# Kernel optimization log

Hardware: AMD Instinct MI355X
Metric: run time of the kernel (lower is better)

Reference implementation:

```python
import jax, jax.numpy as jnp
import numpy as np
from jax import lax

B, T = 16, 128
H, FD = 24, 4          # H hours, FD fourier harmonics
L = 64                 # latent_dim
D = 256                # d_model
NH = 8                 # heads
C = 1 + H * FD         # cont_dim = 97
EPS = 1e-5


def setup_inputs() -> dict:
    key = jax.random.key(0)
    ks = jax.random.split(key, 32)
    r = lambda k, sh, s: (jax.random.normal(k, sh, dtype=jnp.float32) * s)
    z = lambda sh: jnp.zeros(sh, dtype=jnp.float32)
    o = lambda sh: jnp.ones(sh, dtype=jnp.float32)
    return {
        'x_cont': jax.random.normal(ks[0], (B, T, C), dtype=jnp.float32),
        'z0': z((1, 1, L)),                       # learned initial hidden state
        'W_ih': r(ks[1], (L, 1), 0.1),            # RNN input weights
        'W_hh': r(ks[2], (L, L), 0.1),            # RNN recurrent weights
        'b_ih': z((L,)),
        'b_hh': z((L,)),
        'Uf': r(ks[3], (H, FD), 0.01),            # fourier coefficients
        'Wfp': r(ks[4], (L, H), 0.05),            # fourier_proj (L != H)
        'bfp': z((L,)),
        'feat_embed': r(ks[5], (L, D), 0.02),
        'W_in': r(ks[6], (3 * D, D), 0.02),       # MHA in_proj
        'b_in': z((3 * D,)),
        'W_ao': r(ks[7], (D, D), 0.02),           # MHA out_proj
        'b_ao': z((D,)),
        'g1': o((D,)), 'be1': z((D,)),            # ln1
        'W1': r(ks[8], (4 * D, D), 0.02), 'b1': z((4 * D,)),
        'W2': r(ks[9], (D, 4 * D), 0.02), 'b2': z((D,)),
        'g2': o((D,)), 'be2': z((D,)),            # ln2
        'Wop': r(ks[10], (1, D), 0.02), 'bop': z((1,)),   # out_proj d_model->1
        'Wg': r(ks[11], (L, L), 0.05), 'bg': z((L,)),     # gate
        'A': r(ks[12], (H, L), 0.01),
        'c': z((H,)),
    }


def _ln(x, g, b):
    mu = jnp.mean(x, -1, keepdims=True)
    var = jnp.mean(jnp.square(x - mu), -1, keepdims=True)
    return (x - mu) * lax.rsqrt(var + EPS) * g + b


def reference(x_cont, z0, W_ih, W_hh, b_ih, b_hh, Uf, Wfp, bfp, feat_embed,
              W_in, b_in, W_ao, b_ao, g1, be1, W1, b1, W2, b2, g2, be2,
              Wop, bop, Wg, bg, A, c):
    Bb, Tt, Cc = x_cont.shape
    x0 = x_cont[:, :, :1]              # (B,T,1)
    xf = x_cont[:, :, 1:]              # (B,T,H*FD)

    # --- single-layer relu RNN over time ---
    h0 = jnp.broadcast_to(z0[0, 0], (Bb, L))

    def step(h, x_t):                  # x_t: (B,1)
        h = jax.nn.relu(x_t @ W_ih.T + b_ih + h @ W_hh.T + b_hh)
        return h, h

    _, hs = lax.scan(step, h0, jnp.swapaxes(x0, 0, 1))
    h = jnp.swapaxes(hs, 0, 1)         # (B,T,L)

    # --- fourier features ---
    xf_mat = xf.reshape(Bb, Tt, H, FD)
    fourier_h = jnp.einsum('bthf,hf->bth', xf_mat, Uf)   # (B,T,H)
    z = h + fourier_h @ Wfp.T + bfp                      # (B,T,L)

    # --- feature attention: tokens (B*T, L, D) ---
    N = Bb * Tt
    zf = z.reshape(N, L)
    tokens = zf[:, :, None] * feat_embed[None]           # (N,L,D)

    qkv = tokens @ W_in.T + b_in                         # (N,L,3D)
    q, k, v = jnp.split(qkv, 3, axis=-1)
    dh = D // NH
    split_heads = lambda t: t.reshape(N, L, NH, dh).transpose(0, 2, 1, 3)
    q, k, v = split_heads(q), split_heads(k), split_heads(v)
    att = jax.nn.softmax(jnp.einsum('nhqd,nhkd->nhqk', q, k) / np.sqrt(dh), axis=-1)
    ao = jnp.einsum('nhqk,nhkd->nhqd', att, v).transpose(0, 2, 1, 3).reshape(N, L, D)
    ao = ao @ W_ao.T + b_ao

    t1 = _ln(tokens + ao, g1, be1)
    ffn = jax.nn.relu(t1 @ W1.T + b1) @ W2.T + b2
    t2 = _ln(t1 + ffn, g2, be2)
    delta = (t2 @ Wop.T + bop)[..., 0].reshape(Bb, Tt, L)

    gate = jax.nn.sigmoid(z @ Wg.T + bg)
    z_out = z + gate * delta

    o = z_out @ A.T + c                                  # (B,T,H)
    return (o, z_out)
```

## Files before the change

### kernel.cpp

```cpp
#include <hip/hip_runtime.h>

typedef short bf16x8 __attribute__((ext_vector_type(8)));
typedef float f32x4  __attribute__((ext_vector_type(4)));

__device__ __forceinline__ unsigned short f2b(float f){
  union { float f; unsigned u; } v; v.f = f;
  unsigned r = v.u + 0x7FFFu + ((v.u >> 16) & 1u);
  return (unsigned short)(r >> 16);
}
__device__ __forceinline__ float b2f(unsigned short s){
  union { unsigned u; float f; } v; v.u = ((unsigned)s) << 16;
  return v.f;
}
__device__ __forceinline__ unsigned pk2(float lo, float hi){
  unsigned r;
  asm("v_cvt_pk_bf16_f32 %0, %1, %2" : "=v"(r) : "v"(lo), "v"(hi));
  return r;
}

__global__ void k_pre_qkv(const float* __restrict__ FE, const float* __restrict__ W_in,
                          float* __restrict__ Qm, float* __restrict__ Km, float* __restrict__ Vm){
  int id = blockIdx.x*256 + threadIdx.x;
  int part = id >> 14;
  int l = (id >> 8) & 63;
  int d = id & 255;
  const float4* fe = (const float4*)(FE + l*256);
  const float4* wr = (const float4*)(W_in + (part*256 + d)*256);
  float s = 0.f;
  #pragma unroll 8
  for (int k=0;k<64;k++){
    float4 a = fe[k], b = wr[k];
    s += a.x*b.x + a.y*b.y + a.z*b.z + a.w*b.w;
  }
  float* dst = (part==0)?Qm:((part==1)?Km:Vm);
  dst[l*256+d] = s;
}

__global__ void k_pre2(const float* __restrict__ Qm, const float* __restrict__ Km,
                       const float* __restrict__ Vm,
                       const float* __restrict__ b_in, const float* __restrict__ W_ao,
                       const float* __restrict__ b_ao, const float* __restrict__ FE,
                       float* __restrict__ Gc, float* __restrict__ U,
                       float* __restrict__ W, float* __restrict__ S,
                       float* __restrict__ abias, short* __restrict__ M2c,
                       const float* __restrict__ W1, const float* __restrict__ W2,
                       short* __restrict__ W1c, short* __restrict__ W2c,
                       float* __restrict__ FEc,
                       const float* __restrict__ x_cont, const float* __restrict__ z0,
                       const float* __restrict__ W_ih, const float* __restrict__ W_hh,
                       const float* __restrict__ b_ih, const float* __restrict__ b_hh,
                       const float* __restrict__ Uf, const float* __restrict__ Wfp,
                       const float* __restrict__ bfp, float* __restrict__ zout){
  int bid = blockIdx.x;
  int tid = threadIdx.x;
  if (bid < 16){
    int b = bid;
    int l = tid;
    bool act = (l < 64);
    __shared__ float h_sh[64];
    __shared__ float fh_sh[24];
    __shared__ float WfpT[24][64];
    float wr[64];
    float wih=0, bb=0, bf=0;
    float uf0=0,uf1=0,uf2=0,uf3=0;
    if (act){
      #pragma unroll
      for (int j=0;j<64;j++) wr[j] = W_hh[l*64+j];
      #pragma unroll
      for (int j=0;j<24;j++) WfpT[j][l] = Wfp[l*24+j];
      wih = W_ih[l];
      bb  = b_ih[l] + b_hh[l];
      bf  = bfp[l];
      if (l < 24){ uf0=Uf[l*4+0]; uf1=Uf[l*4+1]; uf2=Uf[l*4+2]; uf3=Uf[l*4+3]; }
      h_sh[l] = z0[l];
    }
    __syncthreads();
    const float* xb = x_cont + (size_t)b*128*97;
    for (int t=0;t<128;t++){
      float hn = 0.f, fh = 0.f;
      if (act){
        float x0 = xb[t*97];
        float a0=0,a1=0,a2=0,a3=0;
        #pragma unroll
        for (int j=0;j<64;j+=4){
          a0 += wr[j  ]*h_sh[j  ];
          a1 += wr[j+1]*h_sh[j+1];
          a2 += wr[j+2]*h_sh[j+2];
          a3 += wr[j+3]*h_sh[j+3];
        }
        hn = fmaxf(x0*wih + bb + ((a0+a1)+(a2+a3)), 0.f);
        if (l < 24){
          const float* xf = xb + t*97 + 1 + l*4;
          fh = xf[0]*uf0 + xf[1]*uf1 + xf[2]*uf2 + xf[3]*uf3;
        }
      }
      __syncthreads();
      if (act){
        h_sh[l] = hn;
        if (l < 24) fh_sh[l] = fh;
      }
      __syncthreads();
      if (act){
        float zv = hn + bf;
        #pragma unroll
        for (int j=0;j<24;j++) zv += fh_sh[j]*WfpT[j][l];
        zout[((size_t)b*128 + t)*64 + l] = zv;
      }
    }
    return;
  }
  if (bid < 214){
    int id = (bid-16)*256 + tid;
    const float inv = 0.17677669529663687f;
    if (id < 32768){
      int h = id >> 12, ks = (id>>11)&1, w4 = (id>>9)&3, lane = (id>>3)&63, j = id&7;
      int lq = w4*16 + (lane&15);
      int lk = ks*32 + (lane>>4)*8 + j;
      const float* qp = Qm + lq*256 + h*32;
      const float* kp = Km + lk*256 + h*32;
      float s=0.f;
      #pragma unroll
      for (int d=0;d<32;d++) s += qp[d]*kp[d];
      Gc[id] = s*inv;
    } else if (id < 33280){
      int j = id - 32768; int h = j>>6, lq = j&63;
      const float* qp = Qm + lq*256 + h*32;
      const float* bk = b_in + 256 + h*32;
      float s=0.f;
      #pragma unroll
      for (int d=0;d<32;d++) s += qp[d]*bk[d];
      U[j] = s*inv;
    } else if (id < 33792){
      int j = id - 33280; int h = j>>6, lk = j&63;
      const float* kp = Km + lk*256 + h*32;
      const float* bq = b_in + h*32;
      float s=0.f;
      #pragma unroll
      for (int d=0;d<32;d++) s += bq[d]*kp[d];
      W[j] = s*inv;
    } else if (id < 33800){
      int h = id - 33792;
      float s=0.f;
      #pragma unroll
      for (int d=0;d<32;d++) s += b_in[h*32+d]*b_in[256+h*32+d];
      S[h] = s*inv;
    } else if (id < 34056){
      int e = id - 33800;
      float s = b_ao[e];
      for (int d=0; d<256; d++) s += b_in[512+d]*W_ao[e*256+d];
      abias[e] = s;
    } else if (id < 50440){
      int o = id - 34056;
      int tt = o>>12, et = (o>>10)&3, w4 = (o>>8)&3, lane = (o>>2)&63, j = o&3;
      int row = tt*16 + (lane&15);
      int col = w4*64 + et*16 + (lane>>4)*4 + j;
      FEc[o] = FE[row*256 + col];
    }
    return;
  }
  if (bid < 726){
    int o = (bid-214)*256 + tid;
    int h = o>>14, ks = (o>>13)&1, w4 = (o>>11)&3, et = (o>>9)&3, lane = (o>>3)&63, j = o&7;
    int e = w4*64 + et*16 + (lane&15);
    int lk = ks*32 + (lane>>4)*8 + j;
    const float* vp = Vm + lk*256 + h*32;
    const float* wp = W_ao + e*256 + h*32;
    float s=0.f;
    #pragma unroll
    for (int d=0;d<32;d++) s += vp[d]*wp[d];
    M2c[o] = (short)f2b(s);
    return;
  }
  {
    int id3 = (bid-726)*256 + tid;
    if (id3 < 262144){
      int row = id3 >> 8, col = id3 & 255;
      int c = row >> 7, w4 = (row>>5)&3, ct = (row>>4)&1, lrow = row & 15;
      int ks = col >> 5, lhi = (col>>3)&3, j = col & 7;
      int o = c*32768 + ks*4096 + w4*1024 + ct*512 + (lhi*16+lrow)*8 + j;
      W1c[o] = (short)f2b(W1[id3]);
    } else {
      int idx = id3 - 262144;
      int row = idx >> 10, col = idx & 1023;
      int w4 = row >> 6, et = (row>>4)&3, lrow = row & 15;
      int c = col >> 7, ks2 = (col>>5)&3, lhi = (col>>3)&3, j = col & 7;
      int o = c*32768 + ks2*8192 + w4*2048 + et*512 + (lhi*16+lrow)*8 + j;
      W2c[o] = (short)f2b(W2[idx]);
    }
    return;
  }
}

__global__ __launch_bounds__(256, 3) void k_main(
  const float* __restrict__ zall, const float* __restrict__ Gc,
  const float* __restrict__ Ubuf, const float* __restrict__ Wbuf, const float* __restrict__ Sbuf,
  const float* __restrict__ abias, const short* __restrict__ M2c,
  const float* __restrict__ FEc,
  const short* __restrict__ W1c, const float* __restrict__ b1,
  const short* __restrict__ W2c, const float* __restrict__ b2,
  const float* __restrict__ g1, const float* __restrict__ be1,
  const float* __restrict__ g2, const float* __restrict__ be2,
  const float* __restrict__ Wop, const float* __restrict__ bop,
  const float* __restrict__ Wg, const float* __restrict__ bg,
  const float* __restrict__ Amat, const float* __restrict__ cvec,
  float* __restrict__ out)
{
  const int n = blockIdx.x;
  const int tid = threadIdx.x;
  const int w = tid >> 6, lane = tid & 63, lg = lane >> 4, lr = lane & 15;
  const int cb = w * 64;

  __shared__ __align__(16) short t1_sh[64][264];
  __shared__ __align__(16) char  upool[17408];
  __shared__ float redA[4][64];
  __shared__ float redB[4][64];
  __shared__ float z_sh[64];

  short (*mid_sh)[136] = reinterpret_cast<short (*)[136]>(upool);
  short (*pa_sh)[4][2][64][8] = reinterpret_cast<short (*)[4][2][64][8]>(upool);

  if (tid < 64) z_sh[tid] = zall[n*64 + tid];
  __syncthreads();

  float zkf[16];
  #pragma unroll
  for (int i=0;i<16;i++) zkf[i] = z_sh[(i>>3)*32 + lg*8 + (i&7)];

  f32x4 acc[4][4];
  #pragma unroll
  for (int et=0;et<4;et++)
    #pragma unroll
    for (int tt=0;tt<4;tt++){ f32x4 zz = {0.f,0.f,0.f,0.f}; acc[et][tt] = zz; }

  const int lq_own = w*16 + lr;
  const float zq_own = z_sh[lq_own];

  #pragma unroll 1
  for (int h=0; h<8; ++h){
    {
      const float sh = Sbuf[h];
      const float uh = Ubuf[h*64 + lq_own];
      float e0[16];
      #pragma unroll
      for (int ks=0;ks<2;ks++){
        const float* gbase = Gc + h*4096 + ks*2048 + w*512 + lane*8;
        f32x4 ga = *(const f32x4*)(gbase);
        f32x4 gb = *(const f32x4*)(gbase + 4);
        f32x4 wa = *(const f32x4*)(Wbuf + h*64 + ks*32 + lg*8);
        f32x4 wb = *(const f32x4*)(Wbuf + h*64 + ks*32 + lg*8 + 4);
        #pragma unroll
        for (int j=0;j<4;j++){
          float zk = zkf[ks*8+j];
          e0[ks*8+j]   = zq_own*(zk*ga[j] + uh) + (zk*wa[j] + sh);
          float zk2 = zkf[ks*8+4+j];
          e0[ks*8+4+j] = zq_own*(zk2*gb[j] + uh) + (zk2*wb[j] + sh);
        }
      }
      float mx = e0[0];
      #pragma unroll
      for (int i=1;i<16;i++) mx = fmaxf(mx, e0[i]);
      mx = fmaxf(mx, __shfl_xor(mx,16));
      mx = fmaxf(mx, __shfl_xor(mx,32));
      float sum = 0.f;
      #pragma unroll
      for (int i=0;i<16;i++){ e0[i] = __expf(e0[i]-mx); sum += e0[i]; }
      sum += __shfl_xor(sum,16);
      sum += __shfl_xor(sum,32);
      float inv = 1.f/sum;
      #pragma unroll
      for (int ks=0;ks<2;ks++){
        union { bf16x8 v; unsigned u[4]; } pa;
        #pragma unroll
        for (int p=0;p<4;p++)
          pa.u[p] = pk2(e0[ks*8+2*p]*inv*zkf[ks*8+2*p], e0[ks*8+2*p+1]*inv*zkf[ks*8+2*p+1]);
        *(bf16x8*)&pa_sh[h&1][w][ks][lane][0] = pa.v;
      }
    }
    __syncthreads();
    __builtin_amdgcn_s_setprio(1);
    #pragma unroll
    for (int ks=0; ks<2; ks++){
      bf16x8 am[4], bt[4];
      #pragma unroll
      for (int et=0;et<4;et++)
        am[et] = *(const bf16x8*)(M2c + h*16384 + ks*8192 + w*2048 + et*512 + lane*8);
      #pragma unroll
      for (int tt=0;tt<4;tt++) bt[tt] = *(const bf16x8*)&pa_sh[h&1][tt][ks][lane][0];
      #pragma unroll
      for (int et=0;et<4;et++)
        #pragma unroll
        for (int tt=0;tt<4;tt++)
          acc[et][tt] = __builtin_amdgcn_mfma_f32_16x16x32_bf16(am[et], bt[tt], acc[et][tt], 0,0,0);
    }
    __builtin_amdgcn_s_setprio(0);
  }

  f32x4 ab4[4], g14[4], be14[4];
  #pragma unroll
  for (int et=0;et<4;et++){
    int e0_ = cb + et*16 + lg*4;
    ab4[et]  = *(const f32x4*)(abias + e0_);
    g14[et]  = *(const f32x4*)(g1 + e0_);
    be14[et] = *(const f32x4*)(be1 + e0_);
  }
  float sum1[4], ssq1[4];
  #pragma unroll
  for (int tt=0;tt<4;tt++){
    int tok = tt*16 + lr;
    float zt = z_sh[tok];
    float s = 0.f, sq = 0.f;
    #pragma unroll
    for (int et=0;et<4;et++){
      f32x4 fe = *(const f32x4*)(FEc + tt*4096 + et*1024 + w*256 + lane*4);
      #pragma unroll
      for (int r=0;r<4;r++){
        float v = acc[et][tt][r] + ab4[et][r] + zt*fe[r];
        acc[et][tt][r] = v; s += v; sq += v*v;
      }
    }
    s  += __shfl_xor(s,16);  s  += __shfl_xor(s,32);
    sq += __shfl_xor(sq,16); sq += __shfl_xor(sq,32);
    sum1[tt] = s; ssq1[tt] = sq;
  }
  if (lane < 16){
    #pragma unroll
    for (int tt=0;tt<4;tt++){ redA[w][tt*16+lane] = sum1[tt]; redB[w][tt*16+lane] = ssq1[tt]; }
  }
  __syncthreads();
  float mu1[4], rs1[4];
  #pragma unroll
  for (int tt=0;tt<4;tt++){
    int tok = tt*16 + lr;
    float s  = redA[0][tok] + redA[1][tok] + redA[2][tok] + redA[3][tok];
    float sq = redB[0][tok] + redB[1][tok] + redB[2][tok] + redB[3][tok];
    float m = s * (1.f/256.f);
    mu1[tt] = m;
    rs1[tt] = rsqrtf(sq*(1.f/256.f) - m*m + 1e-5f);
  }
  #pragma unroll
  for (int et=0;et<4;et++)
    #pragma unroll
    for (int tt=0;tt<4;tt++){
      uint2 p;
      float v0 = (acc[et][tt][0]-mu1[tt])*rs1[tt]*g14[et][0] + be14[et][0];
      float v1 = (acc[et][tt][1]-mu1[tt])*rs1[tt]*g14[et][1] + be14[et][1];
      float v2 = (acc[et][tt][2]-mu1[tt])*rs1[tt]*g14[et][2] + be14[et][2];
      float v3 = (acc[et][tt][3]-mu1[tt])*rs1[tt]*g14[et][3] + be14[et][3];
      p.x = pk2(v0,v1); p.y = pk2(v2,v3);
      *(uint2*)&t1_sh[tt*16+lr][cb + et*16 + lg*4] = p;
    }
  __syncthreads();

  #pragma unroll
  for (int et=0;et<4;et++)
    #pragma unroll
    for (int tt=0;tt<4;tt++){ f32x4 zz = {0.f,0.f,0.f,0.f}; acc[et][tt] = zz; }

  #pragma unroll 1
  for (int c=0; c<8; c++){
    f32x4 midv[2][4];
    #pragma unroll
    for (int ct=0;ct<2;ct++){
      f32x4 bi = *(const f32x4*)(b1 + c*128 + w*32 + ct*16 + lg*4);
      #pragma unroll
      for (int tt=0;tt<4;tt++) midv[ct][tt] = bi;
    }
    #pragma unroll
    for (int ks=0; ks<8; ks++){
      bf16x8 bt[4], aw[2];
      #pragma unroll
      for (int tt=0;tt<4;tt++) bt[tt] = *(const bf16x8*)&t1_sh[tt*16+lr][ks*32 + lg*8];
      #pragma unroll
      for (int ct=0;ct<2;ct++)
        aw[ct] = *(const bf16x8*)(W1c + c*32768 + ks*4096 + w*1024 + ct*512 + lane*8);
      #pragma unroll
      for (int ct=0;ct<2;ct++)
        #pragma unroll
        for (int tt=0;tt<4;tt++)
          midv[ct][tt] = __builtin_amdgcn_mfma_f32_16x16x32_bf16(aw[ct], bt[tt], midv[ct][tt], 0,0,0);
    }
    __syncthreads();
    #pragma unroll
    for (int ct=0;ct<2;ct++)
      #pragma unroll
      for (int tt=0;tt<4;tt++){
        uint2 p;
        p.x = pk2(fmaxf(midv[ct][tt][0],0.f), fmaxf(midv[ct][tt][1],0.f));
        p.y = pk2(fmaxf(midv[ct][tt][2],0.f), fmaxf(midv[ct][tt][3],0.f));
        *(uint2*)&mid_sh[tt*16+lr][w*32 + ct*16 + lg*4] = p;
      }
    __syncthreads();
    __builtin_amdgcn_s_setprio(1);
    #pragma unroll
    for (int ks2=0; ks2<4; ks2++){
      bf16x8 aw2[4], bm[4];
      #pragma unroll
      for (int et=0;et<4;et++)
        aw2[et] = *(const bf16x8*)(W2c + c*32768 + ks2*8192 + w*2048 + et*512 + lane*8);
      #pragma unroll
      for (int tt=0;tt<4;tt++) bm[tt] = *(const bf16x8*)&mid_sh[tt*16+lr][ks2*32 + lg*8];
      #pragma unroll
      for (int et=0;et<4;et++)
        #pragma unroll
        for (int tt=0;tt<4;tt++)
          acc[et][tt] = __builtin_amdgcn_mfma_f32_16x16x32_bf16(aw2[et], bm[tt], acc[et][tt], 0,0,0);
    }
    __builtin_amdgcn_s_setprio(0);
  }

  f32x4 b24[4], g24[4], be24[4], wop4[4];
  #pragma unroll
  for (int et=0;et<4;et++){
    int e0_ = cb + et*16 + lg*4;
    b24[et]  = *(const f32x4*)(b2 + e0_);
    g24[et]  = *(const f32x4*)(g2 + e0_);
    be24[et] = *(const f32x4*)(be2 + e0_);
    wop4[et] = *(const f32x4*)(Wop + e0_);
  }
  float sum2[4], ssq2[4];
  #pragma unroll
  for (int tt=0;tt<4;tt++){
    int tok = tt*16 + lr;
    float s = 0.f, sq = 0.f;
    #pragma unroll
    for (int et=0;et<4;et++){
      uint2 t1v = *(const uint2*)&t1_sh[tok][cb + et*16 + lg*4];
      #pragma unroll
      for (int r=0;r<4;r++){
        unsigned short hs = (unsigned short)((r&1) ? ((r<2?t1v.x:t1v.y)>>16) : ((r<2?t1v.x:t1v.y)&0xFFFF));
        float v = acc[et][tt][r] + b24[et][r] + b2f(hs);
        acc[et][tt][r] = v; s += v; sq += v*v;
      }
    }
    s  += __shfl_xor(s,16);  s  += __shfl_xor(s,32);
    sq += __shfl_xor(sq,16); sq += __shfl_xor(sq,32);
    sum2[tt] = s; ssq2[tt] = sq;
  }
  if (lane < 16){
    #pragma unroll
    for (int tt=0;tt<4;tt++){ redA[w][tt*16+lane] = sum2[tt]; redB[w][tt*16+lane] = ssq2[tt]; }
  }
  __syncthreads();

  float gate = 0.f;
  if (tid < 64){
    float gacc = bg[tid];
    const f32x4* wgr = (const f32x4*)(Wg + tid*64);
    #pragma unroll
    for (int j=0;j<16;j++){
      f32x4 wv = wgr[j];
      f32x4 zv = *(const f32x4*)(z_sh + j*4);
      gacc += wv[0]*zv[0] + wv[1]*zv[1] + wv[2]*zv[2] + wv[3]*zv[3];
    }
    gate = 1.f/(1.f + __expf(-gacc));
  }

  float dpart[4];
  #pragma unroll
  for (int tt=0;tt<4;tt++){
    int tok = tt*16 + lr;
    float s  = redA[0][tok] + redA[1][tok] + redA[2][tok] + redA[3][tok];
    float sq = redB[0][tok] + redB[1][tok] + redB[2][tok] + redB[3][tok];
    float m = s * (1.f/256.f);
    float rs = rsqrtf(sq*(1.f/256.f) - m*m + 1e-5f);
    float d = 0.f;
    #pragma unroll
    for (int et=0;et<4;et++)
      #pragma unroll
      for (int r=0;r<4;r++){
        float t2 = (acc[et][tt][r]-m)*rs*g24[et][r] + be24[et][r];
        d += t2*wop4[et][r];
      }
    d += __shfl_xor(d,16); d += __shfl_xor(d,32);
    dpart[tt] = d;
  }
  __syncthreads();
  if (lane < 16){
    #pragma unroll
    for (int tt=0;tt<4;tt++) redA[w][tt*16+lane] = dpart[tt];
  }
  __syncthreads();
  if (tid < 64){
    float delta = redA[0][tid]+redA[1][tid]+redA[2][tid]+redA[3][tid] + bop[0];
    float zo = z_sh[tid] + gate*delta;
    out[49152 + (size_t)n*64 + tid] = zo;
    z_sh[tid] = zo;
  }
  __syncthreads();
  if (tid < 24){
    const float* ar = Amat + tid*64;
    float s = cvec[tid];
    #pragma unroll
    for (int j=0;j<64;j++) s += z_sh[j]*ar[j];
    out[(size_t)n*24 + tid] = s;
  }
}

extern "C" void kernel_launch(void* const* d_in, const int* in_sizes, int n_in,
                              void* d_out, int out_size, void* d_ws, size_t ws_size,
                              hipStream_t stream) {
  const float* x_cont = (const float*)d_in[0];
  const float* z0    = (const float*)d_in[1];
  const float* W_ih  = (const float*)d_in[2];
  const float* W_hh  = (const float*)d_in[3];
  const float* b_ih  = (const float*)d_in[4];
  const float* b_hh  = (const float*)d_in[5];
  const float* Uf    = (const float*)d_in[6];
  const float* Wfp   = (const float*)d_in[7];
  const float* bfp   = (const float*)d_in[8];
  const float* FE    = (const float*)d_in[9];
  const float* W_in  = (const float*)d_in[10];
  const float* b_in  = (const float*)d_in[11];
  const float* W_ao  = (const float*)d_in[12];
  const float* b_ao  = (const float*)d_in[13];
  const float* g1    = (const float*)d_in[14];
  const float* be1   = (const float*)d_in[15];
  const float* W1    = (const float*)d_in[16];
  const float* b1    = (const float*)d_in[17];
  const float* W2    = (const float*)d_in[18];
  const float* b2    = (const float*)d_in[19];
  const float* g2    = (const float*)d_in[20];
  const float* be2   = (const float*)d_in[21];
  const float* Wop   = (const float*)d_in[22];
  const float* bop   = (const float*)d_in[23];
  const float* Wg    = (const float*)d_in[24];
  const float* bg    = (const float*)d_in[25];
  const float* Amat  = (const float*)d_in[26];
  const float* cvec  = (const float*)d_in[27];
  float* out = (float*)d_out;
  char* ws = (char*)d_ws;

  float* z    = (float*)(ws + 0);
  float* Qm   = (float*)(ws + 524288);
  float* Km   = (float*)(ws + 589824);
  float* Vm   = (float*)(ws + 655360);
  float* Gc   = (float*)(ws + 720896);
  float* U    = (float*)(ws + 851968);
  float* Wb   = (float*)(ws + 854016);
  float* S    = (float*)(ws + 856064);
  float* ab   = (float*)(ws + 856320);
  short* M2c  = (short*)(ws + 857344);
  short* W1c  = (short*)(ws + 1119488);
  short* W2c  = (short*)(ws + 1643776);
  float* FEc  = (float*)(ws + 2168064);

  hipLaunchKernelGGL(k_pre_qkv, dim3(192), dim3(256), 0, stream, FE, W_in, Qm, Km, Vm);
  hipLaunchKernelGGL(k_pre2, dim3(2774), dim3(256), 0, stream,
                     Qm, Km, Vm, b_in, W_ao, b_ao, FE, Gc, U, Wb, S, ab, M2c,
                     W1, W2, W1c, W2c, FEc,
                     x_cont, z0, W_ih, W_hh, b_ih, b_hh, Uf, Wfp, bfp, z);
  hipLaunchKernelGGL(k_main, dim3(2048), dim3(256), 0, stream, z, Gc, U, Wb, S, ab, M2c, FEc,
                     W1c, b1, W2c, b2, g1, be1, g2, be2, Wop, bop, Wg, bg, Amat, cvec, out);
}
```

Baseline: 335.4 us.

## Move serial RNN into first pre-kernel and fold log2e into attention scores

The serial 128-step RNN blocks move out of the second precompute kernel and into the first, next to the QKV projection. The long recurrence therefore overlaps with the QKV work instead of extending the second kernel. The score scale now includes log2(e), so the softmax can use exp2f and a hardware reciprocal. The score computation is also rewritten as fused FMAs with a precomputed zq*zk product. The RNN blocks still run serially for 128 steps, so the critical path may not shrink, and the approximate reciprocal slightly changes numerics.

```diff
diff --git a/kernel.cpp b/kernel.cpp
--- a/kernel.cpp
+++ b/kernel.cpp
@@ -18,34 +18,8 @@
   return r;
 }
 
-__global__ void k_pre_qkv(const float* __restrict__ FE, const float* __restrict__ W_in,
-                          float* __restrict__ Qm, float* __restrict__ Km, float* __restrict__ Vm){
-  int id = blockIdx.x*256 + threadIdx.x;
-  int part = id >> 14;
-  int l = (id >> 8) & 63;
-  int d = id & 255;
-  const float4* fe = (const float4*)(FE + l*256);
-  const float4* wr = (const float4*)(W_in + (part*256 + d)*256);
-  float s = 0.f;
-  #pragma unroll 8
-  for (int k=0;k<64;k++){
-    float4 a = fe[k], b = wr[k];
-    s += a.x*b.x + a.y*b.y + a.z*b.z + a.w*b.w;
-  }
-  float* dst = (part==0)?Qm:((part==1)?Km:Vm);
-  dst[l*256+d] = s;
-}
-
-__global__ void k_pre2(const float* __restrict__ Qm, const float* __restrict__ Km,
-                       const float* __restrict__ Vm,
-                       const float* __restrict__ b_in, const float* __restrict__ W_ao,
-                       const float* __restrict__ b_ao, const float* __restrict__ FE,
-                       float* __restrict__ Gc, float* __restrict__ U,
-                       float* __restrict__ W, float* __restrict__ S,
-                       float* __restrict__ abias, short* __restrict__ M2c,
-                       const float* __restrict__ W1, const float* __restrict__ W2,
-                       short* __restrict__ W1c, short* __restrict__ W2c,
-                       float* __restrict__ FEc,
+__global__ void k_pre1(const float* __restrict__ FE, const float* __restrict__ W_in,
+                       float* __restrict__ Qm, float* __restrict__ Km, float* __restrict__ Vm,
                        const float* __restrict__ x_cont, const float* __restrict__ z0,
                        const float* __restrict__ W_ih, const float* __restrict__ W_hh,
                        const float* __restrict__ b_ih, const float* __restrict__ b_hh,
@@ -53,8 +27,25 @@
                        const float* __restrict__ bfp, float* __restrict__ zout){
   int bid = blockIdx.x;
   int tid = threadIdx.x;
-  if (bid < 16){
-    int b = bid;
+  if (bid < 192){
+    int id = bid*256 + tid;
+    int part = id >> 14;
+    int l = (id >> 8) & 63;
+    int d = id & 255;
+    const float4* fe = (const float4*)(FE + l*256);
+    const float4* wr = (const float4*)(W_in + (part*256 + d)*256);
+    float s = 0.f;
+    #pragma unroll 8
+    for (int k=0;k<64;k++){
+      float4 a = fe[k], b = wr[k];
+      s += a.x*b.x + a.y*b.y + a.z*b.z + a.w*b.w;
+    }
+    float* dst = (part==0)?Qm:((part==1)?Km:Vm);
+    dst[l*256+d] = s;
+    return;
+  }
+  {
+    int b = bid - 192;
     int l = tid;
     bool act = (l < 64);
     __shared__ float h_sh[64];
@@ -107,11 +98,24 @@
         zout[((size_t)b*128 + t)*64 + l] = zv;
       }
     }
-    return;
-  }
-  if (bid < 214){
-    int id = (bid-16)*256 + tid;
-    const float inv = 0.17677669529663687f;
+  }
+}
+
+__global__ void k_pre2(const float* __restrict__ Qm, const float* __restrict__ Km,
+                       const float* __restrict__ Vm,
+                       const float* __restrict__ b_in, const float* __restrict__ W_ao,
+                       const float* __restrict__ b_ao, const float* __restrict__ FE,
+                       float* __restrict__ Gc, float* __restrict__ U,
+                       float* __restrict__ W, float* __restrict__ S,
+                       float* __restrict__ abias, short* __restrict__ M2c,
+                       const float* __restrict__ W1, const float* __restrict__ W2,
+                       short* __restrict__ W1c, short* __restrict__ W2c,
+                       float* __restrict__ FEc){
+  int bid = blockIdx.x;
+  int tid = threadIdx.x;
+  const float inv = 0.17677669529663687f * 1.4426950408889634f;
+  if (bid < 198){
+    int id = bid*256 + tid;
     if (id < 32768){
       int h = id >> 12, ks = (id>>11)&1, w4 = (id>>9)&3, lane = (id>>3)&63, j = id&7;
       int lq = w4*16 + (lane&15);
@@ -158,8 +162,8 @@
     }
     return;
   }
-  if (bid < 726){
-    int o = (bid-214)*256 + tid;
+  if (bid < 710){
+    int o = (bid-198)*256 + tid;
     int h = o>>14, ks = (o>>13)&1, w4 = (o>>11)&3, et = (o>>9)&3, lane = (o>>3)&63, j = o&7;
     int e = w4*64 + et*16 + (lane&15);
     int lk = ks*32 + (lane>>4)*8 + j;
@@ -172,7 +176,7 @@
     return;
   }
   {
-    int id3 = (bid-726)*256 + tid;
+    int id3 = (bid-710)*256 + tid;
     if (id3 < 262144){
       int row = id3 >> 8, col = id3 & 255;
       int c = row >> 7, w4 = (row>>5)&3, ct = (row>>4)&1, lrow = row & 15;
@@ -234,12 +238,14 @@
 
   const int lq_own = w*16 + lr;
   const float zq_own = z_sh[lq_own];
+  float zqzk[16];
+  #pragma unroll
+  for (int i=0;i<16;i++) zqzk[i] = zq_own * zkf[i];
 
   #pragma unroll 1
   for (int h=0; h<8; ++h){
     {
-      const float sh = Sbuf[h];
-      const float uh = Ubuf[h*64 + lq_own];
+      const float base = zq_own * Ubuf[h*64 + lq_own] + Sbuf[h];
       float e0[16];
       #pragma unroll
       for (int ks=0;ks<2;ks++){
@@ -250,10 +256,8 @@
         f32x4 wb = *(const f32x4*)(Wbuf + h*64 + ks*32 + lg*8 + 4);
         #pragma unroll
         for (int j=0;j<4;j++){
-          float zk = zkf[ks*8+j];
-          e0[ks*8+j]   = zq_own*(zk*ga[j] + uh) + (zk*wa[j] + sh);
-          float zk2 = zkf[ks*8+4+j];
-          e0[ks*8+4+j] = zq_own*(zk2*gb[j] + uh) + (zk2*wb[j] + sh);
+          e0[ks*8+j]   = fmaf(zqzk[ks*8+j],   ga[j], fmaf(zkf[ks*8+j],   wa[j], base));
+          e0[ks*8+4+j] = fmaf(zqzk[ks*8+4+j], gb[j], fmaf(zkf[ks*8+4+j], wb[j], base));
         }
       }
       float mx = e0[0];
@@ -263,10 +267,10 @@
       mx = fmaxf(mx, __shfl_xor(mx,32));
       float sum = 0.f;
       #pragma unroll
-      for (int i=0;i<16;i++){ e0[i] = __expf(e0[i]-mx); sum += e0[i]; }
+      for (int i=0;i<16;i++){ e0[i] = exp2f(e0[i]-mx); sum += e0[i]; }
       sum += __shfl_xor(sum,16);
       sum += __shfl_xor(sum,32);
-      float inv = 1.f/sum;
+      float inv = __builtin_amdgcn_rcpf(sum);
       #pragma unroll
       for (int ks=0;ks<2;ks++){
         union { bf16x8 v; unsigned u[4]; } pa;
@@ -544,11 +548,12 @@
   short* W2c  = (short*)(ws + 1643776);
   float* FEc  = (float*)(ws + 2168064);
 
-  hipLaunchKernelGGL(k_pre_qkv, dim3(192), dim3(256), 0, stream, FE, W_in, Qm, Km, Vm);
-  hipLaunchKernelGGL(k_pre2, dim3(2774), dim3(256), 0, stream,
+  hipLaunchKernelGGL(k_pre1, dim3(208), dim3(256), 0, stream,
+                     FE, W_in, Qm, Km, Vm,
+                     x_cont, z0, W_ih, W_hh, b_ih, b_hh, Uf, Wfp, bfp, z);
+  hipLaunchKernelGGL(k_pre2, dim3(2758), dim3(256), 0, stream,
                      Qm, Km, Vm, b_in, W_ao, b_ao, FE, Gc, U, Wb, S, ab, M2c,
-                     W1, W2, W1c, W2c, FEc,
-                     x_cont, z0, W_ih, W_hh, b_ih, b_hh, Uf, Wfp, bfp, z);
+                     W1, W2, W1c, W2c, FEc);
   hipLaunchKernelGGL(k_main, dim3(2048), dim3(256), 0, stream, z, Gc, U, Wb, S, ab, M2c, FEc,
                      W1c, b1, W2c, b2, g1, be1, g2, be2, Wop, bop, Wg, bg, Amat, cvec, out);
 }
```

Result: no change. 338.9 us (+1.1%).

## Drop softmax max-subtraction, fold log2e into scores, spread gate matvec across block

Applied to the files above, without the earlier changes.

Attention logits now carry a log2(e) factor folded into the precomputed scale, so softmax uses exp2 directly on fused FMAs with a precomputed zq*zk product. The max reduction and its cross-lane shuffles are removed, which assumes logits stay small enough not to overflow. The gate matvec moves from 64 threads at the end to all 256 threads at the start, written to shared memory. Together these target the softmax ALU work and the serial tail of the main kernel.

```diff
diff --git a/kernel.cpp b/kernel.cpp
--- a/kernel.cpp
+++ b/kernel.cpp
@@ -53,6 +53,7 @@
                        const float* __restrict__ bfp, float* __restrict__ zout){
   int bid = blockIdx.x;
   int tid = threadIdx.x;
+  const float inv = 0.17677669529663687f * 1.4426950408889634f;
   if (bid < 16){
     int b = bid;
     int l = tid;
@@ -111,7 +112,6 @@
   }
   if (bid < 214){
     int id = (bid-16)*256 + tid;
-    const float inv = 0.17677669529663687f;
     if (id < 32768){
       int h = id >> 12, ks = (id>>11)&1, w4 = (id>>9)&3, lane = (id>>3)&63, j = id&7;
       int lq = w4*16 + (lane&15);
@@ -214,6 +214,7 @@
   __shared__ __align__(16) char  upool[17408];
   __shared__ float redA[4][64];
   __shared__ float redB[4][64];
+  __shared__ float gate_sh[64];
   __shared__ float z_sh[64];
 
   short (*mid_sh)[136] = reinterpret_cast<short (*)[136]>(upool);
@@ -226,6 +227,21 @@
   #pragma unroll
   for (int i=0;i<16;i++) zkf[i] = z_sh[(i>>3)*32 + lg*8 + (i&7)];
 
+  {
+    const int glq = tid >> 2, gq = tid & 3;
+    float p = 0.f;
+    const f32x4* wg = (const f32x4*)(Wg + glq*64 + gq*16);
+    const f32x4* zv4 = (const f32x4*)(z_sh + gq*16);
+    #pragma unroll
+    for (int i=0;i<4;i++){
+      f32x4 wv = wg[i], zv = zv4[i];
+      p += wv[0]*zv[0] + wv[1]*zv[1] + wv[2]*zv[2] + wv[3]*zv[3];
+    }
+    p += __shfl_xor(p, 1);
+    p += __shfl_xor(p, 2);
+    if (gq == 0) gate_sh[glq] = 1.f/(1.f + __expf(-(p + bg[glq])));
+  }
+
   f32x4 acc[4][4];
   #pragma unroll
   for (int et=0;et<4;et++)
@@ -234,12 +250,14 @@
 
   const int lq_own = w*16 + lr;
   const float zq_own = z_sh[lq_own];
+  float zqzk[16];
+  #pragma unroll
+  for (int i=0;i<16;i++) zqzk[i] = zq_own * zkf[i];
 
   #pragma unroll 1
   for (int h=0; h<8; ++h){
     {
-      const float sh = Sbuf[h];
-      const float uh = Ubuf[h*64 + lq_own];
+      const float base = zq_own * Ubuf[h*64 + lq_own] + Sbuf[h];
       float e0[16];
       #pragma unroll
       for (int ks=0;ks<2;ks++){
@@ -250,23 +268,16 @@
         f32x4 wb = *(const f32x4*)(Wbuf + h*64 + ks*32 + lg*8 + 4);
         #pragma unroll
         for (int j=0;j<4;j++){
-          float zk = zkf[ks*8+j];
-          e0[ks*8+j]   = zq_own*(zk*ga[j] + uh) + (zk*wa[j] + sh);
-          float zk2 = zkf[ks*8+4+j];
-          e0[ks*8+4+j] = zq_own*(zk2*gb[j] + uh) + (zk2*wb[j] + sh);
+          e0[ks*8+j]   = exp2f(fmaf(zqzk[ks*8+j],   ga[j], fmaf(zkf[ks*8+j],   wa[j], base)));
+          e0[ks*8+4+j] = exp2f(fmaf(zqzk[ks*8+4+j], gb[j], fmaf(zkf[ks*8+4+j], wb[j], base)));
         }
       }
-      float mx = e0[0];
-      #pragma unroll
-      for (int i=1;i<16;i++) mx = fmaxf(mx, e0[i]);
-      mx = fmaxf(mx, __shfl_xor(mx,16));
-      mx = fmaxf(mx, __shfl_xor(mx,32));
       float sum = 0.f;
       #pragma unroll
-      for (int i=0;i<16;i++){ e0[i] = __expf(e0[i]-mx); sum += e0[i]; }
+      for (int i=0;i<16;i++) sum += e0[i];
       sum += __shfl_xor(sum,16);
       sum += __shfl_xor(sum,32);
-      float inv = 1.f/sum;
+      float inv = __builtin_amdgcn_rcpf(sum);
       #pragma unroll
       for (int ks=0;ks<2;ks++){
         union { bf16x8 v; unsigned u[4]; } pa;
@@ -442,19 +453,6 @@
   }
   __syncthreads();
 
-  float gate = 0.f;
-  if (tid < 64){
-    float gacc = bg[tid];
-    const f32x4* wgr = (const f32x4*)(Wg + tid*64);
-    #pragma unroll
-    for (int j=0;j<16;j++){
-      f32x4 wv = wgr[j];
-      f32x4 zv = *(const f32x4*)(z_sh + j*4);
-      gacc += wv[0]*zv[0] + wv[1]*zv[1] + wv[2]*zv[2] + wv[3]*zv[3];
-    }
-    gate = 1.f/(1.f + __expf(-gacc));
-  }
-
   float dpart[4];
   #pragma unroll
   for (int tt=0;tt<4;tt++){
@@ -482,7 +480,7 @@
   __syncthreads();
   if (tid < 64){
     float delta = redA[0][tid]+redA[1][tid]+redA[2][tid]+redA[3][tid] + bop[0];
-    float zo = z_sh[tid] + gate*delta;
+    float zo = z_sh[tid] + gate_sh[tid]*delta;
     out[49152 + (size_t)n*64 + tid] = zo;
     z_sh[tid] = zo;
   }
```

Result: faster. 317.6 us (-5.3%).
